# Performance work log

Measured on AMD Instinct MI355X. Metric: run time of the kernel, lower is better.

The kernel has to match this reference:

```python
import jax, jax.numpy as jnp
import numpy as np

N = 50000; E = 150000
NODE_IN = 16; EDGE_IN = 19; H = 32  # H = max(2*node_in, 32)
LEAK = 0.1; EPS = 1e-5
LAYER_DINS = (16, 32, 32)


def _leaky(x):
    return jnp.where(x >= 0, x, LEAK * x)


def _bn(x, g, b):
    # BatchNorm1d in training mode: batch statistics, biased variance
    m = x.mean(0)
    v = x.var(0)
    return (x - m) * jax.lax.rsqrt(v + EPS) * g + b


def setup_inputs() -> dict:
    key = jax.random.key(0)
    keys = iter(jax.random.split(key, 64))

    def rn(shape, s=0.05):
        return jax.random.normal(next(keys), shape, dtype=jnp.float32) * s

    inp = {
        'x': jax.random.normal(next(keys), (N, NODE_IN), dtype=jnp.float32),
        'edge_index': jax.random.randint(next(keys), (2, E), 0, N),
        'e': jax.random.normal(next(keys), (E, EDGE_IN), dtype=jnp.float32),
        'xbatch': jnp.zeros((N,), dtype=jnp.int32),
        'bn_node_g': jnp.ones((NODE_IN,), jnp.float32), 'bn_node_b': jnp.zeros((NODE_IN,), jnp.float32),
        'bn_edge_g': jnp.ones((EDGE_IN,), jnp.float32), 'bn_edge_b': jnp.zeros((EDGE_IN,), jnp.float32),
    }
    for l, din in enumerate(LAYER_DINS):
        inp[f'l{l}_nnW1'] = rn((EDGE_IN, din));      inp[f'l{l}_nnb1'] = jnp.zeros((din,), jnp.float32)
        inp[f'l{l}_nnW2'] = rn((din, din * H));       inp[f'l{l}_nnb2'] = jnp.zeros((din * H,), jnp.float32)
        inp[f'l{l}_root'] = rn((din, H));             inp[f'l{l}_bias'] = jnp.zeros((H,), jnp.float32)
    # MetaLayer predictor: EdgeModel(H, EDGE_IN, leak) and NodeModel(H, 2, leak)
    inp['em_W1'] = rn((2 * H + EDGE_IN, H)); inp['em_b1'] = jnp.zeros((H,), jnp.float32)
    inp['em_W2'] = rn((H, H));               inp['em_b2'] = jnp.zeros((H,), jnp.float32)
    inp['nm1_W1'] = rn((2 * H, H));          inp['nm1_b1'] = jnp.zeros((H,), jnp.float32)
    inp['nm1_W2'] = rn((H, H));              inp['nm1_b2'] = jnp.zeros((H,), jnp.float32)
    inp['nm2_W1'] = rn((2 * H, H));          inp['nm2_b1'] = jnp.zeros((H,), jnp.float32)
    inp['nm2_W2'] = rn((H, 2));              inp['nm2_b2'] = jnp.zeros((2,), jnp.float32)
    return inp


def _forward(x, e, edge_index, p):
    (bn_node_g, bn_node_b, bn_edge_g, bn_edge_b,
     l0_nnW1, l0_nnb1, l0_nnW2, l0_nnb2, l0_root, l0_bias,
     l1_nnW1, l1_nnb1, l1_nnW2, l1_nnb2, l1_root, l1_bias,
     l2_nnW1, l2_nnb1, l2_nnW2, l2_nnb2, l2_root, l2_bias,
     em_W1, em_b1, em_W2, em_b2,
     nm1_W1, nm1_b1, nm1_W2, nm1_b2,
     nm2_W1, nm2_b1, nm2_W2, nm2_b2) = p

    e = _bn(e, bn_edge_g, bn_edge_b)
    x = _bn(x, bn_node_g, bn_node_b)
    row, col = edge_index[0], edge_index[1]  # source, target (PyG convention)

    layers = [(l0_nnW1, l0_nnb1, l0_nnW2, l0_nnb2, l0_root, l0_bias),
              (l1_nnW1, l1_nnb1, l1_nnW2, l1_nnb2, l1_root, l1_bias),
              (l2_nnW1, l2_nnb1, l2_nnW2, l2_nnb2, l2_root, l2_bias)]
    for (W1, b1, W2, b2, root, bias), din in zip(layers, LAYER_DINS):
        # edge MLP -> per-edge weight matrix [E, din, H]
        w = _leaky(_leaky(e @ W1 + b1) @ W2 + b2).reshape(E, din, H)
        msg = jnp.einsum('ei,eio->eo', x[row], w)              # gather + per-edge matvec
        agg = jax.ops.segment_sum(msg, col, num_segments=N)     # scatter-add ('add' aggr)
        x = agg + x @ root + bias                                # NNConv root weight + bias

    # MetaLayer predictor
    e2 = _leaky(jnp.concatenate([x[row], x[col], e], axis=1) @ em_W1 + em_b1) @ em_W2 + em_b2
    h = _leaky(jnp.concatenate([x[row], e2], axis=1) @ nm1_W1 + nm1_b1) @ nm1_W2 + nm1_b2
    cnt = jnp.clip(jax.ops.segment_sum(jnp.ones((E,), x.dtype), col, num_segments=N), 1.0)
    agg = jax.ops.segment_sum(h, col, num_segments=N) / cnt[:, None]
    xo = _leaky(jnp.concatenate([x, agg], axis=1) @ nm2_W1 + nm2_b1) @ nm2_W2 + nm2_b2
    return jax.nn.log_softmax(xo, axis=1)  # [N, 2] node_pred


def reference(x, edge_index, e, xbatch,
              bn_node_g, bn_node_b, bn_edge_g, bn_edge_b,
              l0_nnW1, l0_nnb1, l0_nnW2, l0_nnb2, l0_root, l0_bias,
              l1_nnW1, l1_nnb1, l1_nnW2, l1_nnb2, l1_root, l1_bias,
              l2_nnW1, l2_nnb1, l2_nnW2, l2_nnb2, l2_root, l2_bias,
              em_W1, em_b1, em_W2, em_b2,
              nm1_W1, nm1_b1, nm1_W2, nm1_b2,
              nm2_W1, nm2_b1, nm2_W2, nm2_b2):
    p = (bn_node_g, bn_node_b, bn_edge_g, bn_edge_b,
         l0_nnW1, l0_nnb1, l0_nnW2, l0_nnb2, l0_root, l0_bias,
         l1_nnW1, l1_nnb1, l1_nnW2, l1_nnb2, l1_root, l1_bias,
         l2_nnW1, l2_nnb1, l2_nnW2, l2_nnb2, l2_root, l2_bias,
         em_W1, em_b1, em_W2, em_b2,
         nm1_W1, nm1_b1, nm1_W2, nm1_b2,
         nm2_W1, nm2_b1, nm2_W2, nm2_b2)
    return _forward(x, e, edge_index, p)
```

## Files before the change

kernel.cpp:

```cpp
#include <hip/hip_runtime.h>
#include <math.h>

constexpr int NN  = 50000;
constexpr int NE  = 150000;
constexpr int NIN = 16;
constexpr int EIN = 19;
constexpr int HD  = 32;
constexpr int NTILES = NE / 16;
constexpr int NBLK_E = 128;
constexpr int NBLK_X = 64;

#define LEAK  0.1f
#define BNEPS 1e-5f

typedef __attribute__((ext_vector_type(8))) short bfrag;
typedef __attribute__((ext_vector_type(4))) float f32x4;
typedef __attribute__((ext_vector_type(2))) float f32x2;
typedef __attribute__((ext_vector_type(4))) int   i32x4;

__device__ __forceinline__ float lky(float v){ return fmaxf(v, LEAK*v); }
__device__ __forceinline__ unsigned f2bf(float f){
  unsigned u = __float_as_uint(f);
  return ((u + 0x7FFFu + ((u >> 16) & 1u)) >> 16);
}
__device__ __forceinline__ void split8(const float* v, i32x4& h4, i32x4& l4){
  unsigned hs[8], ls[8];
  #pragma unroll
  for(int j = 0; j < 8; j++){
    unsigned hh = f2bf(v[j]);
    float hf = __uint_as_float(hh << 16);
    hs[j] = hh; ls[j] = f2bf(v[j] - hf);
  }
  h4[0] = (int)(hs[0] | (hs[1]<<16)); h4[1] = (int)(hs[2] | (hs[3]<<16));
  h4[2] = (int)(hs[4] | (hs[5]<<16)); h4[3] = (int)(hs[6] | (hs[7]<<16));
  l4[0] = (int)(ls[0] | (ls[1]<<16)); l4[1] = (int)(ls[2] | (ls[3]<<16));
  l4[2] = (int)(ls[4] | (ls[5]<<16)); l4[3] = (int)(ls[6] | (ls[7]<<16));
}

__global__ void zero_kernel(float* __restrict__ p, int n){
  int stride = gridDim.x * blockDim.x;
  for(int i = blockIdx.x*blockDim.x + threadIdx.x; i < n; i += stride) p[i] = 0.f;
}

__global__ __launch_bounds__(256) void stats_all_kernel(const float* __restrict__ e,
                                                        const float* __restrict__ x,
                                                        float* __restrict__ partial_e,
                                                        float* __restrict__ partial_x){
  __shared__ float red[4][40];
  const int tid = threadIdx.x, lane = tid & 63, wid = tid >> 6;
  if(blockIdx.x < NBLK_E){
    float s[EIN], q[EIN];
    #pragma unroll
    for(int c = 0; c < EIN; c++){ s[c] = 0.f; q[c] = 0.f; }
    const int gstride = NBLK_E * 256;
    for(int g = blockIdx.x*256 + tid; g < NE/4; g += gstride){
      const f32x4* p = (const f32x4*)(e + (size_t)g * 76);
      #pragma unroll
      for(int m = 0; m < 19; m++){
        f32x4 v = p[m];
        #pragma unroll
        for(int j = 0; j < 4; j++){
          int c = (4*m + j) % 19;
          s[c] += v[j]; q[c] = fmaf(v[j], v[j], q[c]);
        }
      }
    }
    #pragma unroll
    for(int off = 32; off; off >>= 1){
      #pragma unroll
      for(int c = 0; c < EIN; c++){ s[c] += __shfl_xor(s[c], off); q[c] += __shfl_xor(q[c], off); }
    }
    if(lane == 0){
      #pragma unroll
      for(int c = 0; c < EIN; c++){ red[wid][c] = s[c]; red[wid][20 + c] = q[c]; }
    }
    __syncthreads();
    if(tid < 39 && tid != 19)
      partial_e[blockIdx.x*40 + tid] = red[0][tid] + red[1][tid] + red[2][tid] + red[3][tid];
  } else {
    float s[NIN], q[NIN];
    #pragma unroll
    for(int c = 0; c < NIN; c++){ s[c] = 0.f; q[c] = 0.f; }
    const int bid = blockIdx.x - NBLK_E;
    const int gstride = NBLK_X * 256;
    for(int r = bid*256 + tid; r < NN; r += gstride){
      const f32x4* p = (const f32x4*)(x + (size_t)r * NIN);
      #pragma unroll
      for(int m = 0; m < 4; m++){
        f32x4 v = p[m];
        #pragma unroll
        for(int j = 0; j < 4; j++){
          int c = 4*m + j;
          s[c] += v[j]; q[c] = fmaf(v[j], v[j], q[c]);
        }
      }
    }
    #pragma unroll
    for(int off = 32; off; off >>= 1){
      #pragma unroll
      for(int c = 0; c < NIN; c++){ s[c] += __shfl_xor(s[c], off); q[c] += __shfl_xor(q[c], off); }
    }
    if(lane == 0){
      #pragma unroll
      for(int c = 0; c < NIN; c++){ red[wid][c] = s[c]; red[wid][16 + c] = q[c]; }
    }
    __syncthreads();
    if(tid < 32)
      partial_x[bid*32 + tid] = red[0][tid] + red[1][tid] + red[2][tid] + red[3][tid];
  }
}

__global__ __launch_bounds__(1024) void prep_kernel(const float* __restrict__ partial_e,
                                                    const float* __restrict__ partial_x,
                                                    const float* __restrict__ ge, const float* __restrict__ be,
                                                    const float* __restrict__ gx, const float* __restrict__ bx,
                                                    const float* __restrict__ l0W1, const float* __restrict__ l0b1,
                                                    const float* __restrict__ l1W1, const float* __restrict__ l1b1,
                                                    const float* __restrict__ l2W1, const float* __restrict__ l2b1,
                                                    const float* __restrict__ emW1, const float* __restrict__ emb1,
                                                    const float* __restrict__ emW2, const float* __restrict__ emb2,
                                                    const float* __restrict__ nm1W1, const float* __restrict__ nm1b1,
                                                    const float* __restrict__ nm1W2, const float* __restrict__ nm1b2,
                                                    float* __restrict__ ss_g, float* __restrict__ W1f,
                                                    float* __restrict__ b1f, float* __restrict__ biasP,
                                                    short* __restrict__ predpk){
  __shared__ float ss[70];
  __shared__ float emW1f[608];
  __shared__ float emb1f[32];
  __shared__ float predW[7168];
  const int t = threadIdx.x;

  if(t < EIN){
    float s = 0.f, q = 0.f;
    for(int b = 0; b < NBLK_E; b++){ s += partial_e[b*40 + t]; q += partial_e[b*40 + 20 + t]; }
    float m = s / (float)NE;
    float v = q / (float)NE - m*m;
    float sc = ge[t] * rsqrtf(v + BNEPS);
    ss[t] = sc; ss[EIN + t] = be[t] - m*sc;
  } else if(t >= 32 && t < 32 + NIN){
    int c = t - 32;
    float s = 0.f, q = 0.f;
    for(int b = 0; b < NBLK_X; b++){ s += partial_x[b*32 + c]; q += partial_x[b*32 + 16 + c]; }
    float m = s / (float)NN;
    float v = q / (float)NN - m*m;
    float sc = gx[c] * rsqrtf(v + BNEPS);
    ss[2*EIN + c] = sc; ss[2*EIN + NIN + c] = bx[c] - m*sc;
  }
  __syncthreads();
  if(t < 70) ss_g[t] = ss[t];

  if(t < 128){
    int seg = t >> 5, j = t & 31;
    if(seg == 0){
      if(j < NIN){
        float acc = l0b1[j];
        for(int k = 0; k < EIN; k++){
          W1f[0*640 + k*NIN + j] = ss[k] * l0W1[k*NIN + j];
          acc += ss[EIN+k] * l0W1[k*NIN + j];
        }
        b1f[0*32 + j] = acc;
      }
    } else if(seg == 1){
      float acc = l1b1[j];
      for(int k = 0; k < EIN; k++){
        W1f[1*640 + k*HD + j] = ss[k] * l1W1[k*HD + j];
        acc += ss[EIN+k] * l1W1[k*HD + j];
      }
      b1f[1*32 + j] = acc;
    } else if(seg == 2){
      float acc = l2b1[j];
      for(int k = 0; k < EIN; k++){
        W1f[2*640 + k*HD + j] = ss[k] * l2W1[k*HD + j];
        acc += ss[EIN+k] * l2W1[k*HD + j];
      }
      b1f[2*32 + j] = acc;
    } else {
      float acc = emb1[j];
      for(int k = 0; k < EIN; k++){
        emW1f[k*HD + j] = ss[k] * emW1[(2*HD+k)*HD + j];
        acc += ss[EIN+k] * emW1[(2*HD+k)*HD + j];
      }
      emb1f[j] = acc;
    }
  }
  __syncthreads();

  for(int i = t; i < 224*32; i += 1024){
    int k = i >> 5, n = i & 31;
    float v;
    if(k < 64)       v = emW1[k*32 + n];
    else if(k < 83)  v = emW1f[(k-64)*32 + n];
    else if(k < 96)  v = 0.f;
    else if(k < 128) v = emW2[(k-96)*32 + n];
    else if(k < 192) v = nm1W1[(k-128)*32 + n];
    else             v = nm1W2[(k-192)*32 + n];
    predW[i] = v;
  }
  if(t < 128){
    int s = t >> 5, n = t & 31;
    biasP[t] = (s==0) ? emb1f[n] : (s==1) ? emb2[n] : (s==2) ? nm1b1[n] : nm1b2[n];
  }
  __syncthreads();

  for(int idx = t; idx < 14*512; idx += 1024){
    int c = idx >> 9, l = (idx >> 3) & 63, j = idx & 7;
    int kbg = c >> 1, nc = c & 1;
    int k = kbg*32 + 8*(l>>4) + j;
    int n = nc*16 + (l & 15);
    predpk[idx] = (short)f2bf(predW[k*32 + n]);
  }
}

__global__ __launch_bounds__(256) void w2pack_all_kernel(const float* __restrict__ W20,
                                                         const float* __restrict__ W21,
                                                         const float* __restrict__ W22,
                                                         short* __restrict__ w2pk){
  int idx = blockIdx.x*256 + threadIdx.x;
  if(idx >= 81920) return;
  const float* W2; int DIN, base, ci;
  if(idx < 16384){ W2 = W20; DIN = 16; base = 0;     ci = idx; }
  else if(idx < 49152){ W2 = W21; DIN = 32; base = 32768; ci = idx - 16384; }
  else { W2 = W22; DIN = 32; base = 65536; ci = idx - 49152; }
  int c = ci >> 9, l = (ci >> 3) & 63, j = ci & 7;
  int k = 8*(l>>4) + j;
  int n = c*16 + (l & 15);
  float v = (k < DIN) ? W2[(size_t)k*(DIN*HD) + n] : 0.f;
  w2pk[base + ci] = (short)f2bf(v);
}

template<int C>
__global__ void normalize_kernel(const float* __restrict__ in, float* __restrict__ outp,
                                 const float* __restrict__ ss, int rows){
  int n = rows * C;
  int stride = gridDim.x * blockDim.x;
  for(int i = blockIdx.x*blockDim.x + threadIdx.x; i < n; i += stride){
    int c = i % C;
    outp[i] = in[i] * ss[c] + ss[C + c];
  }
}

template<int DIN>
__global__ __launch_bounds__(256) void t1v2_kernel(const float* __restrict__ eraw,
                                                   const float* __restrict__ W1f,
                                                   const float* __restrict__ b1f,
                                                   short* __restrict__ T1){
  int e = blockIdx.x*256 + threadIdx.x;
  if(e >= NE) return;
  const float* ep = eraw + (size_t)e*EIN;
  float eb[EIN];
  #pragma unroll
  for(int k = 0; k < EIN; k++) eb[k] = ep[k];

  float tv[DIN];
  #pragma unroll
  for(int j = 0; j < DIN; j++) tv[j] = b1f[j];
  #pragma unroll
  for(int k = 0; k < EIN; k++){
    float v = eb[k];
    #pragma unroll
    for(int j = 0; j < DIN; j++) tv[j] = fmaf(v, W1f[k*DIN + j], tv[j]);
  }
  unsigned pk[16];
  #pragma unroll
  for(int p = 0; p < 16; p++){
    unsigned lo, hi;
    if(2*p < DIN){ float a = tv[2*p];   lo = f2bf(fmaxf(a, LEAK*a)); } else lo = 0;
    if(2*p+1 < DIN){ float a = tv[2*p+1]; hi = f2bf(fmaxf(a, LEAK*a)); } else hi = 0;
    pk[p] = lo | (hi << 16);
  }
  i32x4* outp = (i32x4*)(T1 + (size_t)e*32);
  #pragma unroll
  for(int g = 0; g < 4; g++){
    i32x4 v; v[0] = (int)pk[g*4]; v[1] = (int)pk[g*4+1]; v[2] = (int)pk[g*4+2]; v[3] = (int)pk[g*4+3];
    outp[g] = v;
  }
}

template<int DIN>
__global__ __launch_bounds__(256) void rootv2_kernel(const float* __restrict__ xin,
                                                     const float* __restrict__ root,
                                                     const float* __restrict__ bias,
                                                     float* __restrict__ xout){
  int n = blockIdx.x*256 + threadIdx.x;
  if(n >= NN) return;
  float xr[DIN];
  const f32x4* xp = (const f32x4*)(xin + (size_t)n*DIN);
  #pragma unroll
  for(int g = 0; g < DIN/4; g++){ f32x4 v = xp[g];
    #pragma unroll
    for(int j = 0; j < 4; j++) xr[g*4+j] = v[j]; }
  float acc[HD];
  #pragma unroll
  for(int o = 0; o < HD; o++) acc[o] = bias[o];
  #pragma unroll
  for(int k = 0; k < DIN; k++){
    float v = xr[k];
    #pragma unroll
    for(int o = 0; o < HD; o++) acc[o] = fmaf(v, root[k*HD + o], acc[o]);
  }
  f32x4* outp = (f32x4*)(xout + (size_t)n*HD);
  #pragma unroll
  for(int g = 0; g < 8; g++){ f32x4 v; v[0]=acc[g*4]; v[1]=acc[g*4+1]; v[2]=acc[g*4+2]; v[3]=acc[g*4+3]; outp[g] = v; }
}

template<int DIN, int NCH, int HALVES>
__global__ __launch_bounds__(512) void msg5_kernel(const short* __restrict__ T1,
                                                   const int* __restrict__ rowp,
                                                   const int* __restrict__ colp,
                                                   const float* __restrict__ xin,
                                                   const short* __restrict__ w2p,
                                                   const float* __restrict__ b2,
                                                   float* __restrict__ xout){
  constexpr int CH  = NCH / HALVES;
  constexpr int XGP = DIN + 1;
  __shared__ short w2s[CH*512];
  __shared__ float b2s[NCH*16];
  __shared__ float xgs[8][16][XGP];

  const int tid = threadIdx.x;
  const int l   = tid & 63;
  const int wid = tid >> 6;
  const int grp = l >> 4, lo16 = l & 15;
  const int tile = blockIdx.x*8 + wid;
  const bool active = tile < NTILES;
  const int e0 = tile * 16;

  if(active){
    int r = rowp[e0 + lo16];
    if(DIN == 32){
      const f32x4* xp = (const f32x4*)(xin + (size_t)r*32 + grp*8);
      *(f32x4*)&xgs[wid][lo16][grp*8]     = xp[0];
      *(f32x4*)&xgs[wid][lo16][grp*8 + 4] = xp[1];
    } else {
      const f32x4* xp = (const f32x4*)(xin + (size_t)r*16 + grp*4);
      *(f32x4*)&xgs[wid][lo16][grp*4] = xp[0];
    }
  }

  bfrag af = {0,0,0,0,0,0,0,0};
  if(active) af = *(const bfrag*)(T1 + (size_t)(e0 + lo16)*32 + grp*8);

  f32x2 m0a = {0.f,0.f}, m0b = {0.f,0.f}, m1a = {0.f,0.f}, m1b = {0.f,0.f};

  for(int h = 0; h < HALVES; h++){
    if(h) __syncthreads();
    for(int t = tid; t < CH*64; t += 512)
      ((i32x4*)w2s)[t] = ((const i32x4*)w2p)[h*CH*64 + t];
    if(h == 0)
      for(int t = tid; t < NCH*16; t += 512) b2s[t] = b2[t];
    __syncthreads();

    if(active){
      #pragma unroll 4
      for(int i = 0; i < CH/2; i++){
        const int cg = h*CH + 2*i;
        const int ig = cg >> 1;
        float bv0 = b2s[cg*16 + lo16];
        float bv1 = b2s[(cg+1)*16 + lo16];
        f32x4 c0 = {bv0,bv0,bv0,bv0};
        f32x4 c1 = {bv1,bv1,bv1,bv1};
        bfrag b0 = *(const bfrag*)&w2s[((2*i  )*64 + l)*8];
        bfrag b1 = *(const bfrag*)&w2s[((2*i+1)*64 + l)*8];
        f32x4 u0 = __builtin_amdgcn_mfma_f32_16x16x32_bf16(af, b0, c0, 0, 0, 0);
        f32x4 u1 = __builtin_amdgcn_mfma_f32_16x16x32_bf16(af, b1, c1, 0, 0, 0);

        f32x2 xva = {xgs[wid][grp*4+0][ig], xgs[wid][grp*4+1][ig]};
        f32x2 xvb = {xgs[wid][grp*4+2][ig], xgs[wid][grp*4+3][ig]};
        f32x2 u0a = {u0[0],u0[1]}, u0b = {u0[2],u0[3]};
        f32x2 u1a = {u1[0],u1[1]}, u1b = {u1[2],u1[3]};
        f32x2 a0a = __builtin_elementwise_max(u0a, u0a*LEAK);
        f32x2 a0b = __builtin_elementwise_max(u0b, u0b*LEAK);
        f32x2 a1a = __builtin_elementwise_max(u1a, u1a*LEAK);
        f32x2 a1b = __builtin_elementwise_max(u1b, u1b*LEAK);
        m0a = __builtin_elementwise_fma(xva, a0a, m0a);
        m0b = __builtin_elementwise_fma(xvb, a0b, m0b);
        m1a = __builtin_elementwise_fma(xva, a1a, m1a);
        m1b = __builtin_elementwise_fma(xvb, a1b, m1b);
      }
    }
  }

  if(active){
    float m0[4] = {m0a[0], m0a[1], m0b[0], m0b[1]};
    float m1[4] = {m1a[0], m1a[1], m1b[0], m1b[1]};
    #pragma unroll
    for(int reg = 0; reg < 4; reg++){
      int ce = colp[e0 + grp*4 + reg];
      atomicAdd(&xout[(size_t)ce*HD + lo16],      m0[reg]);
      atomicAdd(&xout[(size_t)ce*HD + 16 + lo16], m1[reg]);
    }
  }
}

__global__ __launch_bounds__(256) void pred4_kernel(const float* __restrict__ x,
                                                    const float* __restrict__ eraw,
                                                    const int* __restrict__ rowp,
                                                    const int* __restrict__ colp,
                                                    const short* __restrict__ predpk,
                                                    const float* __restrict__ biasP,
                                                    float* __restrict__ agg,
                                                    float* __restrict__ cnt){
  __shared__ short predw[14*512];
  __shared__ float biasl[128];
  __shared__ short fAhi[4][16][104];
  __shared__ short fAlo[4][16][104];
  __shared__ short uAhi[4][16][40];
  __shared__ short uAlo[4][16][40];

  const int tid = threadIdx.x;
  for(int t = tid; t < 14*512/8; t += 256)
    ((i32x4*)predw)[t] = ((const i32x4*)predpk)[t];
  if(tid < 128) biasl[tid] = biasP[tid];
  __syncthreads();

  const int l = tid & 63, wid = tid >> 6;
  const int grp = l >> 4, lo16 = l & 15;
  const int tile = blockIdx.x*4 + wid;
  if(tile >= NTILES) return;
  const int e0 = tile * 16;

  {
    float v[8];
    i32x4 h4, l4;
    int r = rowp[e0 + lo16];
    const float* xp = x + (size_t)r*32 + grp*8;
    #pragma unroll
    for(int j = 0; j < 8; j++) v[j] = xp[j];
    split8(v, h4, l4);
    *(i32x4*)&fAhi[wid][lo16][grp*8] = h4;
    *(i32x4*)&fAlo[wid][lo16][grp*8] = l4;

    int c = colp[e0 + lo16];
    const float* xq = x + (size_t)c*32 + grp*8;
    #pragma unroll
    for(int j = 0; j < 8; j++) v[j] = xq[j];
    split8(v, h4, l4);
    *(i32x4*)&fAhi[wid][lo16][32 + grp*8] = h4;
    *(i32x4*)&fAlo[wid][lo16][32 + grp*8] = l4;

    const float* ep = eraw + (size_t)(e0 + lo16)*EIN;
    #pragma unroll
    for(int j = 0; j < 8; j++){ int f = grp*8 + j; v[j] = (f < EIN) ? ep[f] : 0.f; }
    split8(v, h4, l4);
    *(i32x4*)&fAhi[wid][lo16][64 + grp*8] = h4;
    *(i32x4*)&fAlo[wid][lo16][64 + grp*8] = l4;
  }

  f32x4 z; z[0]=0.f; z[1]=0.f; z[2]=0.f; z[3]=0.f;

  #pragma unroll
  for(int nc = 0; nc < 2; nc++){
    f32x4 acc = z;
    #pragma unroll
    for(int kb = 0; kb < 3; kb++){
      bfrag b  = *(const bfrag*)&predw[((kb*2 + nc)*64 + l)*8];
      bfrag ah = *(const bfrag*)&fAhi[wid][lo16][kb*32 + grp*8];
      bfrag al = *(const bfrag*)&fAlo[wid][lo16][kb*32 + grp*8];
      acc = __builtin_amdgcn_mfma_f32_16x16x32_bf16(ah, b, acc, 0, 0, 0);
      acc = __builtin_amdgcn_mfma_f32_16x16x32_bf16(al, b, acc, 0, 0, 0);
    }
    int n = nc*16 + lo16;
    float bv = biasl[n];
    #pragma unroll
    for(int reg = 0; reg < 4; reg++){
      float uv = acc[reg] + bv; uv = fmaxf(uv, LEAK*uv);
      unsigned hh = f2bf(uv);
      float hf = __uint_as_float(hh << 16);
      uAhi[wid][grp*4 + reg][n] = (short)hh;
      uAlo[wid][grp*4 + reg][n] = (short)f2bf(uv - hf);
    }
  }

  #pragma unroll
  for(int nc = 0; nc < 2; nc++){
    f32x4 acc = z;
    bfrag b  = *(const bfrag*)&predw[((6 + nc)*64 + l)*8];
    bfrag ah = *(const bfrag*)&uAhi[wid][lo16][grp*8];
    bfrag al = *(const bfrag*)&uAlo[wid][lo16][grp*8];
    acc = __builtin_amdgcn_mfma_f32_16x16x32_bf16(ah, b, acc, 0, 0, 0);
    acc = __builtin_amdgcn_mfma_f32_16x16x32_bf16(al, b, acc, 0, 0, 0);
    int n = nc*16 + lo16;
    float bv = biasl[32 + n];
    #pragma unroll
    for(int reg = 0; reg < 4; reg++){
      float ev = acc[reg] + bv;
      unsigned hh = f2bf(ev);
      float hf = __uint_as_float(hh << 16);
      fAhi[wid][grp*4 + reg][32 + n] = (short)hh;
      fAlo[wid][grp*4 + reg][32 + n] = (short)f2bf(ev - hf);
    }
  }

  #pragma unroll
  for(int nc = 0; nc < 2; nc++){
    f32x4 acc = z;
    #pragma unroll
    for(int kb = 0; kb < 2; kb++){
      bfrag b  = *(const bfrag*)&predw[(((4 + kb)*2 + nc)*64 + l)*8];
      bfrag ah = *(const bfrag*)&fAhi[wid][lo16][kb*32 + grp*8];
      bfrag al = *(const bfrag*)&fAlo[wid][lo16][kb*32 + grp*8];
      acc = __builtin_amdgcn_mfma_f32_16x16x32_bf16(ah, b, acc, 0, 0, 0);
      acc = __builtin_amdgcn_mfma_f32_16x16x32_bf16(al, b, acc, 0, 0, 0);
    }
    int n = nc*16 + lo16;
    float bv = biasl[64 + n];
    #pragma unroll
    for(int reg = 0; reg < 4; reg++){
      float vv = acc[reg] + bv; vv = fmaxf(vv, LEAK*vv);
      unsigned hh = f2bf(vv);
      float hf = __uint_as_float(hh << 16);
      uAhi[wid][grp*4 + reg][n] = (short)hh;
      uAlo[wid][grp*4 + reg][n] = (short)f2bf(vv - hf);
    }
  }

  int ce[4];
  #pragma unroll
  for(int reg = 0; reg < 4; reg++) ce[reg] = colp[e0 + grp*4 + reg];

  #pragma unroll
  for(int nc = 0; nc < 2; nc++){
    f32x4 acc = z;
    bfrag b  = *(const bfrag*)&predw[((12 + nc)*64 + l)*8];
    bfrag ah = *(const bfrag*)&uAhi[wid][lo16][grp*8];
    bfrag al = *(const bfrag*)&uAlo[wid][lo16][grp*8];
    acc = __builtin_amdgcn_mfma_f32_16x16x32_bf16(ah, b, acc, 0, 0, 0);
    acc = __builtin_amdgcn_mfma_f32_16x16x32_bf16(al, b, acc, 0, 0, 0);
    int n = nc*16 + lo16;
    float bv = biasl[96 + n];
    #pragma unroll
    for(int reg = 0; reg < 4; reg++)
      atomicAdd(&agg[(size_t)ce[reg]*HD + n], acc[reg] + bv);
  }

  if(l < 16) atomicAdd(&cnt[colp[e0 + l]], 1.f);
}

__global__ __launch_bounds__(256) void final_kernel(const float* __restrict__ x,
                                                    const float* __restrict__ agg,
                                                    const float* __restrict__ cnt,
                                                    const float* __restrict__ W1,
                                                    const float* __restrict__ b1,
                                                    const float* __restrict__ W2,
                                                    const float* __restrict__ b2,
                                                    float* __restrict__ out){
  int n = blockIdx.x*blockDim.x + threadIdx.x;
  if(n >= NN) return;
  float inv = 1.f / fmaxf(cnt[n], 1.f);
  const float* xp = x + (size_t)n * HD;
  const float* ap = agg + (size_t)n * HD;

  float t[HD];
  #pragma unroll
  for(int o = 0; o < HD; o++) t[o] = b1[o];
  #pragma unroll
  for(int k = 0; k < HD; k++){ float v = xp[k]; const float* wp = W1 + k*HD;
    #pragma unroll
    for(int o = 0; o < HD; o++) t[o] += v * wp[o]; }
  #pragma unroll
  for(int k = 0; k < HD; k++){ float v = ap[k] * inv; const float* wp = W1 + (HD+k)*HD;
    #pragma unroll
    for(int o = 0; o < HD; o++) t[o] += v * wp[o]; }

  float a0 = b2[0], a1 = b2[1];
  #pragma unroll
  for(int k = 0; k < HD; k++){ float v = lky(t[k]); a0 += v * W2[k*2]; a1 += v * W2[k*2+1]; }

  float m  = fmaxf(a0, a1);
  float ls = m + logf(expf(a0 - m) + expf(a1 - m));
  out[(size_t)n*2]   = a0 - ls;
  out[(size_t)n*2+1] = a1 - ls;
}

extern "C" void kernel_launch(void* const* d_in, const int* in_sizes, int n_in,
                              void* d_out, int out_size, void* d_ws, size_t ws_size,
                              hipStream_t stream){
  const float* x  = (const float*)d_in[0];
  const int*   ei = (const int*)  d_in[1];
  const float* e  = (const float*)d_in[2];
  const float* bn_node_g = (const float*)d_in[4];
  const float* bn_node_b = (const float*)d_in[5];
  const float* bn_edge_g = (const float*)d_in[6];
  const float* bn_edge_b = (const float*)d_in[7];
  const float* lW1[3], *lb1[3], *lW2[3], *lb2[3], *lroot[3], *lbias[3];
  for(int l = 0; l < 3; l++){
    lW1[l]   = (const float*)d_in[8 + 6*l + 0];
    lb1[l]   = (const float*)d_in[8 + 6*l + 1];
    lW2[l]   = (const float*)d_in[8 + 6*l + 2];
    lb2[l]   = (const float*)d_in[8 + 6*l + 3];
    lroot[l] = (const float*)d_in[8 + 6*l + 4];
    lbias[l] = (const float*)d_in[8 + 6*l + 5];
  }
  const float* emW1  = (const float*)d_in[26];
  const float* emb1  = (const float*)d_in[27];
  const float* emW2  = (const float*)d_in[28];
  const float* emb2  = (const float*)d_in[29];
  const float* nm1W1 = (const float*)d_in[30];
  const float* nm1b1 = (const float*)d_in[31];
  const float* nm1W2 = (const float*)d_in[32];
  const float* nm1b2 = (const float*)d_in[33];
  const float* nm2W1 = (const float*)d_in[34];
  const float* nm2b1 = (const float*)d_in[35];
  const float* nm2W2 = (const float*)d_in[36];
  const float* nm2b2 = (const float*)d_in[37];

  const int* rowp = ei;
  const int* colp = ei + NE;

  float* ws   = (float*)d_ws;
  float* x_bn = ws;
  float* x_a  = x_bn + (size_t)NN*NIN;
  float* x_b  = x_a  + (size_t)NN*HD;
  float* scr  = x_b  + (size_t)NN*HD;
  float* partial_e = scr;
  float* partial_x = scr + 5120;
  float* ss_g      = scr + 7168;
  float* W1f       = scr + 7424;
  float* b1f       = scr + 9344;
  float* biasP     = scr + 9440;
  short* w2pk   = (short*)(scr + 16384);
  short* predpk = w2pk + 3*32768;
  short* T1     = predpk + 8192;
  float* agg    = (float*)T1;
  float* cnt    = agg + (size_t)NN*HD;

  stats_all_kernel<<<NBLK_E + NBLK_X, 256, 0, stream>>>(e, x, partial_e, partial_x);
  prep_kernel<<<1, 1024, 0, stream>>>(partial_e, partial_x,
                                      bn_edge_g, bn_edge_b, bn_node_g, bn_node_b,
                                      lW1[0], lb1[0], lW1[1], lb1[1], lW1[2], lb1[2],
                                      emW1, emb1, emW2, emb2,
                                      nm1W1, nm1b1, nm1W2, nm1b2,
                                      ss_g, W1f, b1f, biasP, predpk);
  w2pack_all_kernel<<<320, 256, 0, stream>>>(lW2[0], lW2[1], lW2[2], w2pk);
  normalize_kernel<NIN><<<1024, 256, 0, stream>>>(x, x_bn, ss_g + 2*EIN, NN);

  const int eblocks = (NE + 255)/256;
  const int nblocks = (NN + 255)/256;
  const int m5blocks = (NTILES + 7)/8;

  rootv2_kernel<NIN><<<nblocks, 256, 0, stream>>>(x_bn, lroot[0], lbias[0], x_a);
  t1v2_kernel<NIN><<<eblocks, 256, 0, stream>>>(e, W1f + 0*640, b1f + 0*32, T1);
  msg5_kernel<NIN, 32, 2><<<m5blocks, 512, 0, stream>>>(T1, rowp, colp, x_bn,
                                                        w2pk + 0*32768, lb2[0], x_a);
  rootv2_kernel<HD><<<nblocks, 256, 0, stream>>>(x_a, lroot[1], lbias[1], x_b);
  t1v2_kernel<HD><<<eblocks, 256, 0, stream>>>(e, W1f + 1*640, b1f + 1*32, T1);
  msg5_kernel<HD, 64, 2><<<m5blocks, 512, 0, stream>>>(T1, rowp, colp, x_a,
                                                       w2pk + 1*32768, lb2[1], x_b);
  rootv2_kernel<HD><<<nblocks, 256, 0, stream>>>(x_b, lroot[2], lbias[2], x_a);
  t1v2_kernel<HD><<<eblocks, 256, 0, stream>>>(e, W1f + 2*640, b1f + 2*32, T1);
  msg5_kernel<HD, 64, 2><<<m5blocks, 512, 0, stream>>>(T1, rowp, colp, x_b,
                                                       w2pk + 2*32768, lb2[2], x_a);

  zero_kernel<<<2048, 256, 0, stream>>>(agg, NN*HD + NN);
  pred4_kernel<<<(NTILES + 3)/4, 256, 0, stream>>>(x_a, e, rowp, colp, predpk, biasP, agg, cnt);
  final_kernel<<<(NN + 255)/256, 256, 0, stream>>>(x_a, agg, cnt,
                                                   nm2W1, nm2b1, nm2W2, nm2b2,
                                                   (float*)d_out);
}
```

Baseline: 269.2 us.

## Fuse edge-MLP first layers, transpose gathered x in LDS, persist pred weights in registers

The three per-layer T1 kernels are merged into one launch that reads the edge features once and writes three separate bf16 buffers. This removes two launches and two extra passes over the edge features, at the cost of extra workspace. The message kernel now stores gathered node features transposed in LDS, so each lane reads them with one vector load instead of strided scalar reads. The prediction kernel keeps its 14 weight fragments and biases in registers and loops over 4 tiles per wave instead of staging weights through LDS in every block. That cuts block count and LDS traffic but raises register pressure.

```diff
diff --git a/kernel.cpp b/kernel.cpp
--- a/kernel.cpp
+++ b/kernel.cpp
@@ -239,11 +239,12 @@
   }
 }
 
-template<int DIN>
-__global__ __launch_bounds__(256) void t1v2_kernel(const float* __restrict__ eraw,
-                                                   const float* __restrict__ W1f,
-                                                   const float* __restrict__ b1f,
-                                                   short* __restrict__ T1){
+__global__ __launch_bounds__(256) void t1all_kernel(const float* __restrict__ eraw,
+                                                    const float* __restrict__ W1f,
+                                                    const float* __restrict__ b1f,
+                                                    short* __restrict__ T10,
+                                                    short* __restrict__ T11,
+                                                    short* __restrict__ T12){
   int e = blockIdx.x*256 + threadIdx.x;
   if(e >= NE) return;
   const float* ep = eraw + (size_t)e*EIN;
@@ -251,28 +252,54 @@
   #pragma unroll
   for(int k = 0; k < EIN; k++) eb[k] = ep[k];
 
-  float tv[DIN];
-  #pragma unroll
-  for(int j = 0; j < DIN; j++) tv[j] = b1f[j];
-  #pragma unroll
-  for(int k = 0; k < EIN; k++){
-    float v = eb[k];
-    #pragma unroll
-    for(int j = 0; j < DIN; j++) tv[j] = fmaf(v, W1f[k*DIN + j], tv[j]);
-  }
-  unsigned pk[16];
-  #pragma unroll
-  for(int p = 0; p < 16; p++){
-    unsigned lo, hi;
-    if(2*p < DIN){ float a = tv[2*p];   lo = f2bf(fmaxf(a, LEAK*a)); } else lo = 0;
-    if(2*p+1 < DIN){ float a = tv[2*p+1]; hi = f2bf(fmaxf(a, LEAK*a)); } else hi = 0;
-    pk[p] = lo | (hi << 16);
-  }
-  i32x4* outp = (i32x4*)(T1 + (size_t)e*32);
-  #pragma unroll
-  for(int g = 0; g < 4; g++){
-    i32x4 v; v[0] = (int)pk[g*4]; v[1] = (int)pk[g*4+1]; v[2] = (int)pk[g*4+2]; v[3] = (int)pk[g*4+3];
-    outp[g] = v;
+  {
+    float tv[16];
+    #pragma unroll
+    for(int j = 0; j < 16; j++) tv[j] = b1f[j];
+    #pragma unroll
+    for(int k = 0; k < EIN; k++){
+      float v = eb[k];
+      #pragma unroll
+      for(int j = 0; j < 16; j++) tv[j] = fmaf(v, W1f[k*16 + j], tv[j]);
+    }
+    unsigned pk[8];
+    #pragma unroll
+    for(int p = 0; p < 8; p++){
+      float a = tv[2*p], b = tv[2*p+1];
+      pk[p] = f2bf(fmaxf(a, LEAK*a)) | (f2bf(fmaxf(b, LEAK*b)) << 16);
+    }
+    i32x4* outp = (i32x4*)(T10 + (size_t)e*32);
+    i32x4 v0; v0[0]=(int)pk[0]; v0[1]=(int)pk[1]; v0[2]=(int)pk[2]; v0[3]=(int)pk[3];
+    i32x4 v1; v1[0]=(int)pk[4]; v1[1]=(int)pk[5]; v1[2]=(int)pk[6]; v1[3]=(int)pk[7];
+    i32x4 zz; zz[0]=0; zz[1]=0; zz[2]=0; zz[3]=0;
+    outp[0] = v0; outp[1] = v1; outp[2] = zz; outp[3] = zz;
+  }
+  #pragma unroll
+  for(int l = 1; l < 3; l++){
+    const float* Wl = W1f + l*640;
+    const float* bl = b1f + l*32;
+    short* Tl = (l == 1) ? T11 : T12;
+    float tv[32];
+    #pragma unroll
+    for(int j = 0; j < 32; j++) tv[j] = bl[j];
+    #pragma unroll
+    for(int k = 0; k < EIN; k++){
+      float v = eb[k];
+      #pragma unroll
+      for(int j = 0; j < 32; j++) tv[j] = fmaf(v, Wl[k*32 + j], tv[j]);
+    }
+    unsigned pk[16];
+    #pragma unroll
+    for(int p = 0; p < 16; p++){
+      float a = tv[2*p], b = tv[2*p+1];
+      pk[p] = f2bf(fmaxf(a, LEAK*a)) | (f2bf(fmaxf(b, LEAK*b)) << 16);
+    }
+    i32x4* outp = (i32x4*)(Tl + (size_t)e*32);
+    #pragma unroll
+    for(int g = 0; g < 4; g++){
+      i32x4 v; v[0]=(int)pk[g*4]; v[1]=(int)pk[g*4+1]; v[2]=(int)pk[g*4+2]; v[3]=(int)pk[g*4+3];
+      outp[g] = v;
+    }
   }
 }
 
@@ -304,18 +331,17 @@
 }
 
 template<int DIN, int NCH, int HALVES>
-__global__ __launch_bounds__(512) void msg5_kernel(const short* __restrict__ T1,
+__global__ __launch_bounds__(512) void msg6_kernel(const short* __restrict__ T1,
                                                    const int* __restrict__ rowp,
                                                    const int* __restrict__ colp,
                                                    const float* __restrict__ xin,
                                                    const short* __restrict__ w2p,
                                                    const float* __restrict__ b2,
                                                    float* __restrict__ xout){
-  constexpr int CH  = NCH / HALVES;
-  constexpr int XGP = DIN + 1;
+  constexpr int CH = NCH / HALVES;
   __shared__ short w2s[CH*512];
   __shared__ float b2s[NCH*16];
-  __shared__ float xgs[8][16][XGP];
+  __shared__ float xgs[8][DIN][16];
 
   const int tid = threadIdx.x;
   const int l   = tid & 63;
@@ -329,11 +355,16 @@
     int r = rowp[e0 + lo16];
     if(DIN == 32){
       const f32x4* xp = (const f32x4*)(xin + (size_t)r*32 + grp*8);
-      *(f32x4*)&xgs[wid][lo16][grp*8]     = xp[0];
-      *(f32x4*)&xgs[wid][lo16][grp*8 + 4] = xp[1];
+      f32x4 a = xp[0], b = xp[1];
+      #pragma unroll
+      for(int j = 0; j < 4; j++) xgs[wid][grp*8 + j][lo16]     = a[j];
+      #pragma unroll
+      for(int j = 0; j < 4; j++) xgs[wid][grp*8 + 4 + j][lo16] = b[j];
     } else {
       const f32x4* xp = (const f32x4*)(xin + (size_t)r*16 + grp*4);
-      *(f32x4*)&xgs[wid][lo16][grp*4] = xp[0];
+      f32x4 a = xp[0];
+      #pragma unroll
+      for(int j = 0; j < 4; j++) xgs[wid][grp*4 + j][lo16] = a[j];
     }
   }
 
@@ -364,8 +395,8 @@
         f32x4 u0 = __builtin_amdgcn_mfma_f32_16x16x32_bf16(af, b0, c0, 0, 0, 0);
         f32x4 u1 = __builtin_amdgcn_mfma_f32_16x16x32_bf16(af, b1, c1, 0, 0, 0);
 
-        f32x2 xva = {xgs[wid][grp*4+0][ig], xgs[wid][grp*4+1][ig]};
-        f32x2 xvb = {xgs[wid][grp*4+2][ig], xgs[wid][grp*4+3][ig]};
+        f32x4 xv = *(const f32x4*)&xgs[wid][ig][grp*4];
+        f32x2 xva = {xv[0], xv[1]}, xvb = {xv[2], xv[3]};
         f32x2 u0a = {u0[0],u0[1]}, u0b = {u0[2],u0[3]};
         f32x2 u1a = {u1[0],u1[1]}, u1b = {u1[2],u1[3]};
         f32x2 a0a = __builtin_elementwise_max(u0a, u0a*LEAK);
@@ -392,148 +423,151 @@
   }
 }
 
-__global__ __launch_bounds__(256) void pred4_kernel(const float* __restrict__ x,
-                                                    const float* __restrict__ eraw,
-                                                    const int* __restrict__ rowp,
-                                                    const int* __restrict__ colp,
-                                                    const short* __restrict__ predpk,
-                                                    const float* __restrict__ biasP,
-                                                    float* __restrict__ agg,
-                                                    float* __restrict__ cnt){
-  __shared__ short predw[14*512];
-  __shared__ float biasl[128];
+__global__ __launch_bounds__(256, 4) void pred5_kernel(const float* __restrict__ x,
+                                                       const float* __restrict__ eraw,
+                                                       const int* __restrict__ rowp,
+                                                       const int* __restrict__ colp,
+                                                       const short* __restrict__ predpk,
+                                                       const float* __restrict__ biasP,
+                                                       float* __restrict__ agg,
+                                                       float* __restrict__ cnt){
   __shared__ short fAhi[4][16][104];
   __shared__ short fAlo[4][16][104];
   __shared__ short uAhi[4][16][40];
   __shared__ short uAlo[4][16][40];
 
   const int tid = threadIdx.x;
-  for(int t = tid; t < 14*512/8; t += 256)
-    ((i32x4*)predw)[t] = ((const i32x4*)predpk)[t];
-  if(tid < 128) biasl[tid] = biasP[tid];
-  __syncthreads();
-
   const int l = tid & 63, wid = tid >> 6;
   const int grp = l >> 4, lo16 = l & 15;
-  const int tile = blockIdx.x*4 + wid;
-  if(tile >= NTILES) return;
-  const int e0 = tile * 16;
-
-  {
-    float v[8];
-    i32x4 h4, l4;
-    int r = rowp[e0 + lo16];
-    const float* xp = x + (size_t)r*32 + grp*8;
-    #pragma unroll
-    for(int j = 0; j < 8; j++) v[j] = xp[j];
-    split8(v, h4, l4);
-    *(i32x4*)&fAhi[wid][lo16][grp*8] = h4;
-    *(i32x4*)&fAlo[wid][lo16][grp*8] = l4;
-
-    int c = colp[e0 + lo16];
-    const float* xq = x + (size_t)c*32 + grp*8;
-    #pragma unroll
-    for(int j = 0; j < 8; j++) v[j] = xq[j];
-    split8(v, h4, l4);
-    *(i32x4*)&fAhi[wid][lo16][32 + grp*8] = h4;
-    *(i32x4*)&fAlo[wid][lo16][32 + grp*8] = l4;
-
-    const float* ep = eraw + (size_t)(e0 + lo16)*EIN;
-    #pragma unroll
-    for(int j = 0; j < 8; j++){ int f = grp*8 + j; v[j] = (f < EIN) ? ep[f] : 0.f; }
-    split8(v, h4, l4);
-    *(i32x4*)&fAhi[wid][lo16][64 + grp*8] = h4;
-    *(i32x4*)&fAlo[wid][lo16][64 + grp*8] = l4;
+
+  bfrag wb[14];
+  #pragma unroll
+  for(int c = 0; c < 14; c++) wb[c] = *(const bfrag*)(predpk + ((size_t)c*64 + l)*8);
+  float bP[8];
+  #pragma unroll
+  for(int s = 0; s < 4; s++){
+    bP[s*2]   = biasP[s*32 + lo16];
+    bP[s*2+1] = biasP[s*32 + 16 + lo16];
   }
 
   f32x4 z; z[0]=0.f; z[1]=0.f; z[2]=0.f; z[3]=0.f;
-
-  #pragma unroll
-  for(int nc = 0; nc < 2; nc++){
-    f32x4 acc = z;
-    #pragma unroll
-    for(int kb = 0; kb < 3; kb++){
-      bfrag b  = *(const bfrag*)&predw[((kb*2 + nc)*64 + l)*8];
-      bfrag ah = *(const bfrag*)&fAhi[wid][lo16][kb*32 + grp*8];
-      bfrag al = *(const bfrag*)&fAlo[wid][lo16][kb*32 + grp*8];
-      acc = __builtin_amdgcn_mfma_f32_16x16x32_bf16(ah, b, acc, 0, 0, 0);
-      acc = __builtin_amdgcn_mfma_f32_16x16x32_bf16(al, b, acc, 0, 0, 0);
-    }
-    int n = nc*16 + lo16;
-    float bv = biasl[n];
-    #pragma unroll
-    for(int reg = 0; reg < 4; reg++){
-      float uv = acc[reg] + bv; uv = fmaxf(uv, LEAK*uv);
-      unsigned hh = f2bf(uv);
-      float hf = __uint_as_float(hh << 16);
-      uAhi[wid][grp*4 + reg][n] = (short)hh;
-      uAlo[wid][grp*4 + reg][n] = (short)f2bf(uv - hf);
-    }
-  }
-
-  #pragma unroll
-  for(int nc = 0; nc < 2; nc++){
-    f32x4 acc = z;
-    bfrag b  = *(const bfrag*)&predw[((6 + nc)*64 + l)*8];
-    bfrag ah = *(const bfrag*)&uAhi[wid][lo16][grp*8];
-    bfrag al = *(const bfrag*)&uAlo[wid][lo16][grp*8];
-    acc = __builtin_amdgcn_mfma_f32_16x16x32_bf16(ah, b, acc, 0, 0, 0);
-    acc = __builtin_amdgcn_mfma_f32_16x16x32_bf16(al, b, acc, 0, 0, 0);
-    int n = nc*16 + lo16;
-    float bv = biasl[32 + n];
-    #pragma unroll
-    for(int reg = 0; reg < 4; reg++){
-      float ev = acc[reg] + bv;
-      unsigned hh = f2bf(ev);
-      float hf = __uint_as_float(hh << 16);
-      fAhi[wid][grp*4 + reg][32 + n] = (short)hh;
-      fAlo[wid][grp*4 + reg][32 + n] = (short)f2bf(ev - hf);
-    }
-  }
-
-  #pragma unroll
-  for(int nc = 0; nc < 2; nc++){
-    f32x4 acc = z;
-    #pragma unroll
-    for(int kb = 0; kb < 2; kb++){
-      bfrag b  = *(const bfrag*)&predw[(((4 + kb)*2 + nc)*64 + l)*8];
-      bfrag ah = *(const bfrag*)&fAhi[wid][lo16][kb*32 + grp*8];
-      bfrag al = *(const bfrag*)&fAlo[wid][lo16][kb*32 + grp*8];
-      acc = __builtin_amdgcn_mfma_f32_16x16x32_bf16(ah, b, acc, 0, 0, 0);
-      acc = __builtin_amdgcn_mfma_f32_16x16x32_bf16(al, b, acc, 0, 0, 0);
-    }
-    int n = nc*16 + lo16;
-    float bv = biasl[64 + n];
-    #pragma unroll
-    for(int reg = 0; reg < 4; reg++){
-      float vv = acc[reg] + bv; vv = fmaxf(vv, LEAK*vv);
-      unsigned hh = f2bf(vv);
-      float hf = __uint_as_float(hh << 16);
-      uAhi[wid][grp*4 + reg][n] = (short)hh;
-      uAlo[wid][grp*4 + reg][n] = (short)f2bf(vv - hf);
-    }
-  }
-
-  int ce[4];
-  #pragma unroll
-  for(int reg = 0; reg < 4; reg++) ce[reg] = colp[e0 + grp*4 + reg];
-
-  #pragma unroll
-  for(int nc = 0; nc < 2; nc++){
-    f32x4 acc = z;
-    bfrag b  = *(const bfrag*)&predw[((12 + nc)*64 + l)*8];
-    bfrag ah = *(const bfrag*)&uAhi[wid][lo16][grp*8];
-    bfrag al = *(const bfrag*)&uAlo[wid][lo16][grp*8];
-    acc = __builtin_amdgcn_mfma_f32_16x16x32_bf16(ah, b, acc, 0, 0, 0);
-    acc = __builtin_amdgcn_mfma_f32_16x16x32_bf16(al, b, acc, 0, 0, 0);
-    int n = nc*16 + lo16;
-    float bv = biasl[96 + n];
-    #pragma unroll
-    for(int reg = 0; reg < 4; reg++)
-      atomicAdd(&agg[(size_t)ce[reg]*HD + n], acc[reg] + bv);
-  }
-
-  if(l < 16) atomicAdd(&cnt[colp[e0 + l]], 1.f);
+  const int tbase = (blockIdx.x*4 + wid) * 4;
+
+  for(int tt = 0; tt < 4; tt++){
+    const int tile = tbase + tt;
+    if(tile >= NTILES) break;
+    const int e0 = tile * 16;
+
+    {
+      float v[8];
+      i32x4 h4, l4;
+      int r = rowp[e0 + lo16];
+      const float* xp = x + (size_t)r*32 + grp*8;
+      #pragma unroll
+      for(int j = 0; j < 8; j++) v[j] = xp[j];
+      split8(v, h4, l4);
+      *(i32x4*)&fAhi[wid][lo16][grp*8] = h4;
+      *(i32x4*)&fAlo[wid][lo16][grp*8] = l4;
+
+      int c = colp[e0 + lo16];
+      const float* xq = x + (size_t)c*32 + grp*8;
+      #pragma unroll
+      for(int j = 0; j < 8; j++) v[j] = xq[j];
+      split8(v, h4, l4);
+      *(i32x4*)&fAhi[wid][lo16][32 + grp*8] = h4;
+      *(i32x4*)&fAlo[wid][lo16][32 + grp*8] = l4;
+
+      const float* ep = eraw + (size_t)(e0 + lo16)*EIN;
+      #pragma unroll
+      for(int j = 0; j < 8; j++){ int f = grp*8 + j; v[j] = (f < EIN) ? ep[f] : 0.f; }
+      split8(v, h4, l4);
+      *(i32x4*)&fAhi[wid][lo16][64 + grp*8] = h4;
+      *(i32x4*)&fAlo[wid][lo16][64 + grp*8] = l4;
+    }
+
+    #pragma unroll
+    for(int nc = 0; nc < 2; nc++){
+      f32x4 acc = z;
+      #pragma unroll
+      for(int kb = 0; kb < 3; kb++){
+        bfrag ah = *(const bfrag*)&fAhi[wid][lo16][kb*32 + grp*8];
+        bfrag al = *(const bfrag*)&fAlo[wid][lo16][kb*32 + grp*8];
+        acc = __builtin_amdgcn_mfma_f32_16x16x32_bf16(ah, wb[kb*2 + nc], acc, 0, 0, 0);
+        acc = __builtin_amdgcn_mfma_f32_16x16x32_bf16(al, wb[kb*2 + nc], acc, 0, 0, 0);
+      }
+      int n = nc*16 + lo16;
+      float bv = bP[nc];
+      #pragma unroll
+      for(int reg = 0; reg < 4; reg++){
+        float uv = acc[reg] + bv; uv = fmaxf(uv, LEAK*uv);
+        unsigned hh = f2bf(uv);
+        float hf = __uint_as_float(hh << 16);
+        uAhi[wid][grp*4 + reg][n] = (short)hh;
+        uAlo[wid][grp*4 + reg][n] = (short)f2bf(uv - hf);
+      }
+    }
+
+    #pragma unroll
+    for(int nc = 0; nc < 2; nc++){
+      f32x4 acc = z;
+      bfrag ah = *(const bfrag*)&uAhi[wid][lo16][grp*8];
+      bfrag al = *(const bfrag*)&uAlo[wid][lo16][grp*8];
+      acc = __builtin_amdgcn_mfma_f32_16x16x32_bf16(ah, wb[6 + nc], acc, 0, 0, 0);
+      acc = __builtin_amdgcn_mfma_f32_16x16x32_bf16(al, wb[6 + nc], acc, 0, 0, 0);
+      int n = nc*16 + lo16;
+      float bv = bP[2 + nc];
+      #pragma unroll
+      for(int reg = 0; reg < 4; reg++){
+        float ev = acc[reg] + bv;
+        unsigned hh = f2bf(ev);
+        float hf = __uint_as_float(hh << 16);
+        fAhi[wid][grp*4 + reg][32 + n] = (short)hh;
+        fAlo[wid][grp*4 + reg][32 + n] = (short)f2bf(ev - hf);
+      }
+    }
+
+    #pragma unroll
+    for(int nc = 0; nc < 2; nc++){
+      f32x4 acc = z;
+      #pragma unroll
+      for(int kb = 0; kb < 2; kb++){
+        bfrag ah = *(const bfrag*)&fAhi[wid][lo16][kb*32 + grp*8];
+        bfrag al = *(const bfrag*)&fAlo[wid][lo16][kb*32 + grp*8];
+        acc = __builtin_amdgcn_mfma_f32_16x16x32_bf16(ah, wb[8 + kb*2 + nc], acc, 0, 0, 0);
+        acc = __builtin_amdgcn_mfma_f32_16x16x32_bf16(al, wb[8 + kb*2 + nc], acc, 0, 0, 0);
+      }
+      int n = nc*16 + lo16;
+      float bv = bP[4 + nc];
+      #pragma unroll
+      for(int reg = 0; reg < 4; reg++){
+        float vv = acc[reg] + bv; vv = fmaxf(vv, LEAK*vv);
+        unsigned hh = f2bf(vv);
+        float hf = __uint_as_float(hh << 16);
+        uAhi[wid][grp*4 + reg][n] = (short)hh;
+        uAlo[wid][grp*4 + reg][n] = (short)f2bf(vv - hf);
+      }
+    }
+
+    int ce[4];
+    #pragma unroll
+    for(int reg = 0; reg < 4; reg++) ce[reg] = colp[e0 + grp*4 + reg];
+
+    #pragma unroll
+    for(int nc = 0; nc < 2; nc++){
+      f32x4 acc = z;
+      bfrag ah = *(const bfrag*)&uAhi[wid][lo16][grp*8];
+      bfrag al = *(const bfrag*)&uAlo[wid][lo16][grp*8];
+      acc = __builtin_amdgcn_mfma_f32_16x16x32_bf16(ah, wb[12 + nc], acc, 0, 0, 0);
+      acc = __builtin_amdgcn_mfma_f32_16x16x32_bf16(al, wb[12 + nc], acc, 0, 0, 0);
+      int n = nc*16 + lo16;
+      float bv = bP[6 + nc];
+      #pragma unroll
+      for(int reg = 0; reg < 4; reg++)
+        atomicAdd(&agg[(size_t)ce[reg]*HD + n], acc[reg] + bv);
+    }
+
+    if(l < 16) atomicAdd(&cnt[colp[e0 + l]], 1.f);
+  }
 }
 
 __global__ __launch_bounds__(256) void final_kernel(const float* __restrict__ x,
@@ -620,8 +654,10 @@
   float* biasP     = scr + 9440;
   short* w2pk   = (short*)(scr + 16384);
   short* predpk = w2pk + 3*32768;
-  short* T1     = predpk + 8192;
-  float* agg    = (float*)T1;
+  short* T10    = predpk + 8192;
+  short* T11    = T10 + (size_t)NE*32;
+  short* T12    = T11 + (size_t)NE*32;
+  float* agg    = (float*)T10;
   float* cnt    = agg + (size_t)NN*HD;
 
   stats_all_kernel<<<NBLK_E + NBLK_X, 256, 0, stream>>>(e, x, partial_e, partial_x);
@@ -633,26 +669,23 @@
                                       ss_g, W1f, b1f, biasP, predpk);
   w2pack_all_kernel<<<320, 256, 0, stream>>>(lW2[0], lW2[1], lW2[2], w2pk);
   normalize_kernel<NIN><<<1024, 256, 0, stream>>>(x, x_bn, ss_g + 2*EIN, NN);
-
-  const int eblocks = (NE + 255)/256;
-  const int nblocks = (NN + 255)/256;
-  const int m5blocks = (NTILES + 7)/8;
+  t1all_kernel<<<(NE + 255)/256, 256, 0, stream>>>(e, W1f, b1f, T10, T11, T12);
+
+  const int nblocks  = (NN + 255)/256;
+  const int m6blocks = (NTILES + 7)/8;
 
   rootv2_kernel<NIN><<<nblocks, 256, 0, stream>>>(x_bn, lroot[0], lbias[0], x_a);
-  t1v2_kernel<NIN><<<eblocks, 256, 0, stream>>>(e, W1f + 0*640, b1f + 0*32, T1);
-  msg5_kernel<NIN, 32, 2><<<m5blocks, 512, 0, stream>>>(T1, rowp, colp, x_bn,
+  msg6_kernel<NIN, 32, 2><<<m6blocks, 512, 0, stream>>>(T10, rowp, colp, x_bn,
                                                         w2pk + 0*32768, lb2[0], x_a);
   rootv2_kernel<HD><<<nblocks, 256, 0, stream>>>(x_a, lroot[1], lbias[1], x_b);
-  t1v2_kernel<HD><<<eblocks, 256, 0, stream>>>(e, W1f + 1*640, b1f + 1*32, T1);
-  msg5_kernel<HD, 64, 2><<<m5blocks, 512, 0, stream>>>(T1, rowp, colp, x_a,
+  msg6_kernel<HD, 64, 2><<<m6blocks, 512, 0, stream>>>(T11, rowp, colp, x_a,
                                                        w2pk + 1*32768, lb2[1], x_b);
   rootv2_kernel<HD><<<nblocks, 256, 0, stream>>>(x_b, lroot[2], lbias[2], x_a);
-  t1v2_kernel<HD><<<eblocks, 256, 0, stream>>>(e, W1f + 2*640, b1f + 2*32, T1);
-  msg5_kernel<HD, 64, 2><<<m5blocks, 512, 0, stream>>>(T1, rowp, colp, x_b,
+  msg6_kernel<HD, 64, 2><<<m6blocks, 512, 0, stream>>>(T12, rowp, colp, x_b,
                                                        w2pk + 2*32768, lb2[2], x_a);
 
   zero_kernel<<<2048, 256, 0, stream>>>(agg, NN*HD + NN);
-  pred4_kernel<<<(NTILES + 3)/4, 256, 0, stream>>>(x_a, e, rowp, colp, predpk, biasP, agg, cnt);
+  pred5_kernel<<<(NTILES + 15)/16, 256, 0, stream>>>(x_a, e, rowp, colp, predpk, biasP, agg, cnt);
   final_kernel<<<(NN + 255)/256, 256, 0, stream>>>(x_a, agg, cnt,
                                                    nm2W1, nm2b1, nm2W2, nm2b2,
                                                    (float*)d_out);
```

Result: faster. 246.2 us (-8.5%).
